# Performance work log

Measured on AMD Instinct MI355X. Metric: run time of the kernel, lower is better.

The kernel has to match this reference:

```python
import jax, jax.numpy as jnp
import numpy as np

IMAGE_SIZE = 512


def _build_masks(image_size):
    # Vectorized equivalent of the module's triple-loop pyramid construction.
    w = h = image_size
    x = w - 1  # pyramid is (w-1, h-1)
    idx = np.arange(x)
    J, K = np.meshgrid(idx, idx, indexing='ij')
    # ring index i at (j,k) is min distance to any border of the (x,x) square
    ring = np.minimum(np.minimum(J, K), np.minimum(x - 1 - J, x - 1 - K))
    pyramid = x // 2 - ring
    plane = np.full((w, h), w // 2, dtype=np.int64)
    plane[1:, 1:] = pyramid
    L = image_size // 2 + 1  # number of bins
    # one-hot rectangular-ring masks: mask[r] = (plane == r)
    mask = (plane[None, :, :] == np.arange(L)[:, None, None]).astype(np.float32)
    mask_n = np.maximum(mask.sum(axis=(1, 2)), 1e-8).astype(np.float32)
    return jnp.asarray(mask), jnp.asarray(mask_n)


def setup_inputs() -> dict:
    key = jax.random.key(0)
    x = jax.random.uniform(key, (16, 3, IMAGE_SIZE, IMAGE_SIZE), dtype=jnp.float32)
    mask, mask_n = _build_masks(IMAGE_SIZE)
    return {"x": x, "mask": mask, "mask_n": mask_n}


def reference(x, mask, mask_n):
    # only_psd=True branch: RGB -> luma, scaled by 20
    mag = 20.0 * (0.299 * x[:, 0] + 0.587 * x[:, 1] + 0.114 * x[:, 2])  # [B,H,W]
    # per-bin masked average; einsum avoids materializing [B,L,H,W]
    profile = jnp.einsum('bhw,lhw->bl', mag, mask) / mask_n  # [B,L]
    pmin = profile.min()
    pmax = profile.max()
    return (profile - pmin) / (pmax - pmin)
```

## Files before the change

kernel.cpp:

```cpp
#include <hip/hip_runtime.h>

#define IMG 512
#define HW (IMG * IMG)
#define NB 257
#define BATCH 16
#define RG 128


__global__ __launch_bounds__(256, 8) void hist_kernel(const float* __restrict__ x,
                                                      float* __restrict__ partial) {
    const int gx   = blockIdx.x;
    const int b    = blockIdx.y;
    const int wid  = threadIdx.x >> 6;
    const int lane = threadIdx.x & 63;

    __shared__ float bins[NB];
    for (int i = threadIdx.x; i < NB; i += 256) bins[i] = 0.f;
    __syncthreads();

    const int h = (gx << 2) + wid;
    const float* xr  = x + (size_t)b * 3 * HW + (size_t)h * IMG;
    const float* xg  = xr + HW;
    const float* xbl = xg + HW;

    const int wA = (lane << 2);
    const int wB = wA + 256;

    const float4 rA = *reinterpret_cast<const float4*>(xr  + wA);
    const float4 gA = *reinterpret_cast<const float4*>(xg  + wA);
    const float4 bA = *reinterpret_cast<const float4*>(xbl + wA);
    const float4 rB = *reinterpret_cast<const float4*>(xr  + wB);
    const float4 gB = *reinterpret_cast<const float4*>(xg  + wB);
    const float4 bB = *reinterpret_cast<const float4*>(xbl + wB);

    float mgA[4], mgB[4];
    mgA[0] = 20.f * (0.299f * rA.x + 0.587f * gA.x + 0.114f * bA.x);
    mgA[1] = 20.f * (0.299f * rA.y + 0.587f * gA.y + 0.114f * bA.y);
    mgA[2] = 20.f * (0.299f * rA.z + 0.587f * gA.z + 0.114f * bA.z);
    mgA[3] = 20.f * (0.299f * rA.w + 0.587f * gA.w + 0.114f * bA.w);
    mgB[0] = 20.f * (0.299f * rB.x + 0.587f * gB.x + 0.114f * bB.x);
    mgB[1] = 20.f * (0.299f * rB.y + 0.587f * gB.y + 0.114f * bB.y);
    mgB[2] = 20.f * (0.299f * rB.z + 0.587f * gB.z + 0.114f * bB.z);
    mgB[3] = 20.f * (0.299f * rB.w + 0.587f * gB.w + 0.114f * bB.w);

    const int m = min(h - 1, 511 - h);
    float mid = 0.f;

    if (h == 0) {
        mid = mgA[0] + mgA[1] + mgA[2] + mgA[3] +
              mgB[0] + mgB[1] + mgB[2] + mgB[3];
    } else {
#pragma unroll
        for (int t = 0; t < 4; ++t) {
            const int w = wA + t;
            if (w == 0) {
                atomicAdd(&bins[256], mgA[t]);
            } else {
                const int d = min(w - 1, 511 - w);
                if (d >= m) mid += mgA[t];
                else        atomicAdd(&bins[255 - d], mgA[t]);
            }
        }
#pragma unroll
        for (int t = 0; t < 4; ++t) {
            const int w = wB + t;
            const int d = min(w - 1, 511 - w);
            if (d >= m) mid += mgB[t];
            else        atomicAdd(&bins[255 - d], mgB[t]);
        }
    }

#pragma unroll
    for (int off = 32; off > 0; off >>= 1) mid += __shfl_down(mid, off, 64);
    if (lane == 0) atomicAdd(&bins[(h == 0) ? 256 : (255 - m)], mid);
    __syncthreads();

    float* pp = partial + ((size_t)b * RG + gx) * NB;
    for (int i = threadIdx.x; i < NB; i += 256) pp[i] = bins[i];
}

__global__ __launch_bounds__(256) void reduce_kernel(const float* __restrict__ partial,
                                                     const float* __restrict__ mask_n,
                                                     float* __restrict__ profile) {
    const int b = blockIdx.x;
    const float* p0 = partial + (size_t)b * RG * NB;
    for (int l = threadIdx.x; l < NB; l += 256) {
        float s = 0.f;
#pragma unroll 8
        for (int g = 0; g < RG; ++g) s += p0[(size_t)g * NB + l];
        profile[b * NB + l] = s / mask_n[l];
    }
}

__global__ __launch_bounds__(1024) void norm_kernel(const float* __restrict__ profile,
                                                    float* __restrict__ out) {
    __shared__ float red_min[16];
    __shared__ float red_max[16];
    const int lane = threadIdx.x & 63;
    const int wv   = threadIdx.x >> 6;

    float lmin = 3.402823466e+38f, lmax = -3.402823466e+38f;
    float v[5];
#pragma unroll
    for (int k = 0; k < 5; ++k) {
        const int i = threadIdx.x + (k << 10);
        v[k] = (i < BATCH * NB) ? profile[i] : profile[0];
        lmin = fminf(lmin, v[k]);
        lmax = fmaxf(lmax, v[k]);
    }
#pragma unroll
    for (int off = 32; off > 0; off >>= 1) {
        lmin = fminf(lmin, __shfl_xor(lmin, off, 64));
        lmax = fmaxf(lmax, __shfl_xor(lmax, off, 64));
    }
    if (lane == 0) { red_min[wv] = lmin; red_max[wv] = lmax; }
    __syncthreads();

    float pmin = red_min[0], pmax = red_max[0];
#pragma unroll
    for (int k = 1; k < 16; ++k) {
        pmin = fminf(pmin, red_min[k]);
        pmax = fmaxf(pmax, red_max[k]);
    }
    const float inv = 1.f / (pmax - pmin);
#pragma unroll
    for (int k = 0; k < 5; ++k) {
        const int i = threadIdx.x + (k << 10);
        if (i < BATCH * NB) out[i] = (v[k] - pmin) * inv;
    }
}

extern "C" void kernel_launch(void* const* d_in, const int* in_sizes, int n_in,
                              void* d_out, int out_size, void* d_ws, size_t ws_size,
                              hipStream_t stream) {
    const float* x      = (const float*)d_in[0];
    const float* mask_n = (const float*)d_in[2];
    float* out     = (float*)d_out;
    float* partial = (float*)d_ws;
    float* profile = partial + (size_t)BATCH * RG * NB;

    hist_kernel<<<dim3(RG, BATCH), 256, 0, stream>>>(x, partial);
    reduce_kernel<<<BATCH, 256, 0, stream>>>(partial, mask_n, profile);
    norm_kernel<<<1, 1024, 0, stream>>>(profile, out);
}
```

Measured before the change: 41.99 us.

## Coarsen histogram blocks to 32 rows and fuse reduce with normalization

```diff
diff --git a/kernel.cpp b/kernel.cpp
--- a/kernel.cpp
+++ b/kernel.cpp
@@ -4,96 +4,91 @@
 #define HW (IMG * IMG)
 #define NB 257
 #define BATCH 16
-#define RG 128
+#define GX 16
+#define RPB 32
+#define THREADS 512
 
 
-__global__ __launch_bounds__(256, 8) void hist_kernel(const float* __restrict__ x,
-                                                      float* __restrict__ partial) {
+__global__ __launch_bounds__(THREADS) void hist_kernel(const float* __restrict__ x,
+                                                       float* __restrict__ partial) {
     const int gx   = blockIdx.x;
     const int b    = blockIdx.y;
     const int wid  = threadIdx.x >> 6;
     const int lane = threadIdx.x & 63;
 
     __shared__ float bins[NB];
-    for (int i = threadIdx.x; i < NB; i += 256) bins[i] = 0.f;
+    for (int i = threadIdx.x; i < NB; i += THREADS) bins[i] = 0.f;
     __syncthreads();
 
-    const int h = (gx << 2) + wid;
-    const float* xr  = x + (size_t)b * 3 * HW + (size_t)h * IMG;
-    const float* xg  = xr + HW;
-    const float* xbl = xg + HW;
-
+    const float* xbase = x + (size_t)b * 3 * HW;
+    const int h0 = gx * RPB + (wid << 2);
     const int wA = (lane << 2);
     const int wB = wA + 256;
 
-    const float4 rA = *reinterpret_cast<const float4*>(xr  + wA);
-    const float4 gA = *reinterpret_cast<const float4*>(xg  + wA);
-    const float4 bA = *reinterpret_cast<const float4*>(xbl + wA);
-    const float4 rB = *reinterpret_cast<const float4*>(xr  + wB);
-    const float4 gB = *reinterpret_cast<const float4*>(xg  + wB);
-    const float4 bB = *reinterpret_cast<const float4*>(xbl + wB);
+#pragma unroll
+    for (int rr = 0; rr < 4; ++rr) {
+        const int h = h0 + rr;
+        const float* xr  = xbase + (size_t)h * IMG;
+        const float* xg  = xr + HW;
+        const float* xbl = xg + HW;
 
-    float mgA[4], mgB[4];
-    mgA[0] = 20.f * (0.299f * rA.x + 0.587f * gA.x + 0.114f * bA.x);
-    mgA[1] = 20.f * (0.299f * rA.y + 0.587f * gA.y + 0.114f * bA.y);
-    mgA[2] = 20.f * (0.299f * rA.z + 0.587f * gA.z + 0.114f * bA.z);
-    mgA[3] = 20.f * (0.299f * rA.w + 0.587f * gA.w + 0.114f * bA.w);
-    mgB[0] = 20.f * (0.299f * rB.x + 0.587f * gB.x + 0.114f * bB.x);
-    mgB[1] = 20.f * (0.299f * rB.y + 0.587f * gB.y + 0.114f * bB.y);
-    mgB[2] = 20.f * (0.299f * rB.z + 0.587f * gB.z + 0.114f * bB.z);
-    mgB[3] = 20.f * (0.299f * rB.w + 0.587f * gB.w + 0.114f * bB.w);
+        const float4 rA = *reinterpret_cast<const float4*>(xr  + wA);
+        const float4 gA = *reinterpret_cast<const float4*>(xg  + wA);
+        const float4 bA = *reinterpret_cast<const float4*>(xbl + wA);
+        const float4 rB = *reinterpret_cast<const float4*>(xr  + wB);
+        const float4 gB = *reinterpret_cast<const float4*>(xg  + wB);
+        const float4 bB = *reinterpret_cast<const float4*>(xbl + wB);
 
-    const int m = min(h - 1, 511 - h);
-    float mid = 0.f;
+        float mgA[4], mgB[4];
+        mgA[0] = 20.f * (0.299f * rA.x + 0.587f * gA.x + 0.114f * bA.x);
+        mgA[1] = 20.f * (0.299f * rA.y + 0.587f * gA.y + 0.114f * bA.y);
+        mgA[2] = 20.f * (0.299f * rA.z + 0.587f * gA.z + 0.114f * bA.z);
+        mgA[3] = 20.f * (0.299f * rA.w + 0.587f * gA.w + 0.114f * bA.w);
+        mgB[0] = 20.f * (0.299f * rB.x + 0.587f * gB.x + 0.114f * bB.x);
+        mgB[1] = 20.f * (0.299f * rB.y + 0.587f * gB.y + 0.114f * bB.y);
+        mgB[2] = 20.f * (0.299f * rB.z + 0.587f * gB.z + 0.114f * bB.z);
+        mgB[3] = 20.f * (0.299f * rB.w + 0.587f * gB.w + 0.114f * bB.w);
 
-    if (h == 0) {
-        mid = mgA[0] + mgA[1] + mgA[2] + mgA[3] +
-              mgB[0] + mgB[1] + mgB[2] + mgB[3];
-    } else {
+        const int m = min(h - 1, 511 - h);
+        float mid = 0.f;
+
+        if (h == 0) {
+            mid = mgA[0] + mgA[1] + mgA[2] + mgA[3] +
+                  mgB[0] + mgB[1] + mgB[2] + mgB[3];
+        } else {
 #pragma unroll
-        for (int t = 0; t < 4; ++t) {
-            const int w = wA + t;
-            if (w == 0) {
-                atomicAdd(&bins[256], mgA[t]);
-            } else {
+            for (int t = 0; t < 4; ++t) {
+                const int w = wA + t;
+                if (w == 0) {
+                    atomicAdd(&bins[256], mgA[t]);
+                } else {
+                    const int d = min(w - 1, 511 - w);
+                    if (d >= m) mid += mgA[t];
+                    else        atomicAdd(&bins[255 - d], mgA[t]);
+                }
+            }
+#pragma unroll
+            for (int t = 0; t < 4; ++t) {
+                const int w = wB + t;
                 const int d = min(w - 1, 511 - w);
-                if (d >= m) mid += mgA[t];
-                else        atomicAdd(&bins[255 - d], mgA[t]);
+                if (d >= m) mid += mgB[t];
+                else        atomicAdd(&bins[255 - d], mgB[t]);
             }
         }
-#pragma unroll
-        for (int t = 0; t < 4; ++t) {
-            const int w = wB + t;
-            const int d = min(w - 1, 511 - w);
-            if (d >= m) mid += mgB[t];
-            else        atomicAdd(&bins[255 - d], mgB[t]);
-        }
-    }
 
 #pragma unroll
-    for (int off = 32; off > 0; off >>= 1) mid += __shfl_down(mid, off, 64);
-    if (lane == 0) atomicAdd(&bins[(h == 0) ? 256 : (255 - m)], mid);
+        for (int off = 32; off > 0; off >>= 1) mid += __shfl_down(mid, off, 64);
+        if (lane == 0) atomicAdd(&bins[(h == 0) ? 256 : (255 - m)], mid);
+    }
     __syncthreads();
 
-    float* pp = partial + ((size_t)b * RG + gx) * NB;
-    for (int i = threadIdx.x; i < NB; i += 256) pp[i] = bins[i];
+    float* pp = partial + ((size_t)b * GX + gx) * NB;
+    for (int i = threadIdx.x; i < NB; i += THREADS) pp[i] = bins[i];
 }
 
-__global__ __launch_bounds__(256) void reduce_kernel(const float* __restrict__ partial,
-                                                     const float* __restrict__ mask_n,
-                                                     float* __restrict__ profile) {
-    const int b = blockIdx.x;
-    const float* p0 = partial + (size_t)b * RG * NB;
-    for (int l = threadIdx.x; l < NB; l += 256) {
-        float s = 0.f;
-#pragma unroll 8
-        for (int g = 0; g < RG; ++g) s += p0[(size_t)g * NB + l];
-        profile[b * NB + l] = s / mask_n[l];
-    }
-}
-
-__global__ __launch_bounds__(1024) void norm_kernel(const float* __restrict__ profile,
-                                                    float* __restrict__ out) {
+__global__ __launch_bounds__(1024) void finalize_kernel(const float* __restrict__ partial,
+                                                        const float* __restrict__ mask_n,
+                                                        float* __restrict__ out) {
     __shared__ float red_min[16];
     __shared__ float red_max[16];
     const int lane = threadIdx.x & 63;
@@ -104,9 +99,20 @@
 #pragma unroll
     for (int k = 0; k < 5; ++k) {
         const int i = threadIdx.x + (k << 10);
-        v[k] = (i < BATCH * NB) ? profile[i] : profile[0];
-        lmin = fminf(lmin, v[k]);
-        lmax = fmaxf(lmax, v[k]);
+        if (i < BATCH * NB) {
+            const int bb = i / NB;
+            const int l  = i - bb * NB;
+            const float* p = partial + (size_t)bb * GX * NB + l;
+            float s = 0.f;
+#pragma unroll
+            for (int g = 0; g < GX; ++g) s += p[(size_t)g * NB];
+            s /= mask_n[l];
+            v[k] = s;
+            lmin = fminf(lmin, s);
+            lmax = fmaxf(lmax, s);
+        } else {
+            v[k] = 0.f;
+        }
     }
 #pragma unroll
     for (int off = 32; off > 0; off >>= 1) {
@@ -137,9 +143,7 @@
     const float* mask_n = (const float*)d_in[2];
     float* out     = (float*)d_out;
     float* partial = (float*)d_ws;
-    float* profile = partial + (size_t)BATCH * RG * NB;
 
-    hist_kernel<<<dim3(RG, BATCH), 256, 0, stream>>>(x, partial);
-    reduce_kernel<<<BATCH, 256, 0, stream>>>(partial, mask_n, profile);
-    norm_kernel<<<1, 1024, 0, stream>>>(profile, out);
+    hist_kernel<<<dim3(GX, BATCH), THREADS, 0, stream>>>(x, partial);
+    finalize_kernel<<<1, 1024, 0, stream>>>(partial, mask_n, out);
 }
```

New measurement: 35.31 us (median of 2 runs). -15.9%, faster.
